# Performance work log

Measured on AMD Instinct MI355X. Metric: run time of the kernel, lower is better.

The kernel has to match this reference:

```python
import jax, jax.numpy as jnp
import numpy as np

B, S, OBS, ZD, HID, T, PD = 256, 512, 64, 16, 256, 64, 2
ITERS, ELITES = 4, 64
SMOOTH, STD_FLOOR = 0.25, 0.2
IW, AW, RW = 1.0, 0.5, 1.0


def setup_inputs() -> dict:
    key = jax.random.key(0)
    ks = jax.random.split(key, 32)
    f32 = jnp.float32

    def w(k, shape):
        return jax.random.normal(k, shape, f32) / np.float32(np.sqrt(shape[0]))

    return {
        "s0": jax.random.normal(ks[0], (B, OBS), f32),
        "eps": jax.random.normal(ks[1], (ITERS, B, S, ZD), f32),
        "enc_w1": w(ks[2], (OBS, HID)), "enc_b1": jnp.zeros((HID,), f32),
        "enc_w2": w(ks[3], (HID, HID)), "enc_b2": jnp.zeros((HID,), f32),
        "zmu_w": w(ks[4], (HID, ZD)), "zmu_b": jnp.zeros((ZD,), f32),
        "zls_w": w(ks[5], (HID, ZD)), "zls_b": jnp.zeros((ZD,), f32),
        "mu_w1": w(ks[6], (OBS + ZD, HID)), "mu_b1": jnp.zeros((HID,), f32),
        "mu_w2": w(ks[7], (HID, HID)), "mu_b2": jnp.zeros((HID,), f32),
        "mu_w3": w(ks[8], (HID, T * PD)), "mu_b3": jnp.zeros((T * PD,), f32),
        "sig_w1": w(ks[9], (ZD, HID)), "sig_b1": jnp.zeros((HID,), f32),
        "sig_w2": w(ks[10], (HID, HID)), "sig_b2": jnp.zeros((HID,), f32),
        "sig_w3": w(ks[11], (HID, T * PD)), "sig_b3": jnp.zeros((T * PD,), f32),  # bias zero-init per nn.init.zeros_
        "risk_w1": w(ks[12], (OBS + ZD, HID)), "risk_b1": jnp.zeros((HID,), f32),
        "risk_w2": w(ks[13], (HID, HID)), "risk_b2": jnp.zeros((HID,), f32),
        "risk_w3": w(ks[14], (HID, 1)), "risk_b3": jnp.zeros((1,), f32),
    }


def _cem_bind(s0, eps, enc_w1, enc_b1, enc_w2, enc_b2, zmu_w, zmu_b, zls_w, zls_b,
              mu_w1, mu_b1, mu_w2, mu_b2, mu_w3, mu_b3,
              sig_w1, sig_b1, sig_w2, sig_b2, sig_w3, sig_b3,
              risk_w1, risk_b1, risk_w2, risk_b2, risk_w3, risk_b3):
    relu = jax.nn.relu
    b, obs = s0.shape
    iters, _, s, zd = eps.shape

    # --- TubeNet.encode: q(z|s0) ---
    h = relu(s0 @ enc_w1 + enc_b1)
    h = relu(h @ enc_w2 + enc_b2)
    mu = h @ zmu_w + zmu_b                                   # [B, ZD]
    std = jnp.exp(jnp.clip(h @ zls_w + zls_b, -4.0, 2.0))    # [B, ZD]

    goal = s0[:, 2:4]                                        # extract_goal
    s0e = jnp.broadcast_to(s0[:, None, :], (b, s, obs))      # [B, S, OBS]

    best_score = jnp.full((b,), -jnp.inf, dtype=s0.dtype)
    best_z = mu

    for i in range(iters):  # small fixed CEM iteration count
        z = mu[:, None, :] + std[:, None, :] * eps[i]        # [B, S, ZD]
        x = jnp.concatenate([s0e, z], axis=-1)               # [B, S, OBS+ZD]

        # predict_tube: mu_net(s0, z)
        hm = relu(x @ mu_w1 + mu_b1)
        hm = relu(hm @ mu_w2 + mu_b2)
        mu_out = (hm @ mu_w3 + mu_b3).reshape(b, s, T, PD)

        # sigma_net(z), clamp(-4, 3); agency = -mean(log sigma) = -mean(logsig)
        hs = relu(z @ sig_w1 + sig_b1)
        hs = relu(hs @ sig_w2 + sig_b2)
        logsig = jnp.clip(hs @ sig_w3 + sig_b3, -4.0, 3.0)   # [B, S, T*PD]

        # intent proxy: ||mu_T - goal||^2
        intent = jnp.sum((mu_out[:, :, -1, :] - goal[:, None, :]) ** 2, axis=-1)  # [B, S]
        agency = -jnp.mean(logsig, axis=-1)                  # [B, S]

        # RiskNet(s0, z)
        hr = relu(x @ risk_w1 + risk_b1)
        hr = relu(hr @ risk_w2 + risk_b2)
        risk = jax.nn.sigmoid(hr @ risk_w3 + risk_b3)[..., 0]  # [B, S]

        score = -IW * intent + AW * agency - RW * risk       # [B, S]

        vals, idx = jax.lax.top_k(score, ELITES)             # [B, E]
        elite_z = jnp.take_along_axis(z, idx[:, :, None], axis=1)  # [B, E, ZD]

        better = vals[:, 0] > best_score
        top_z = jnp.take_along_axis(z, idx[:, :1, None], axis=1)[:, 0, :]
        best_score = jnp.where(better, vals[:, 0], best_score)
        best_z = jnp.where(better[:, None], top_z, best_z)

        new_mu = elite_z.mean(axis=1)
        new_std = jnp.std(elite_z, axis=1, ddof=1)           # torch .std default (unbiased)
        mu = SMOOTH * mu + (1.0 - SMOOTH) * new_mu
        std = jnp.maximum(SMOOTH * std + (1.0 - SMOOTH) * new_std, STD_FLOOR)

    return jnp.concatenate([best_z, best_score[:, None]], axis=-1)  # [B, ZD+1]


def reference(s0, eps, enc_w1, enc_b1, enc_w2, enc_b2, zmu_w, zmu_b, zls_w, zls_b,
              mu_w1, mu_b1, mu_w2, mu_b2, mu_w3, mu_b3,
              sig_w1, sig_b1, sig_w2, sig_b2, sig_w3, sig_b3,
              risk_w1, risk_b1, risk_w2, risk_b2, risk_w3, risk_b3):
    return _cem_bind(s0, eps, enc_w1, enc_b1, enc_w2, enc_b2, zmu_w, zmu_b, zls_w, zls_b,
                     mu_w1, mu_b1, mu_w2, mu_b2, mu_w3, mu_b3,
                     sig_w1, sig_b1, sig_w2, sig_b2, sig_w3, sig_b3,
                     risk_w1, risk_b1, risk_w2, risk_b2, risk_w3, risk_b3)
```

## Files before the change

kernel.cpp:

```cpp
#include <hip/hip_runtime.h>

#define B_    256
#define S_    512
#define OBS_  64
#define ZD_   16
#define HID_  256
#define ITERS_ 4
#define RT_   16
#define STR_  20

__global__ __launch_bounds__(256) void enc_kernel(
    const float* __restrict__ s0,
    const float* __restrict__ w1, const float* __restrict__ b1,
    const float* __restrict__ w2, const float* __restrict__ b2,
    const float* __restrict__ zmw, const float* __restrict__ zmb,
    const float* __restrict__ zlw, const float* __restrict__ zlb,
    const float* __restrict__ mu_w1, const float* __restrict__ mu_b1,
    const float* __restrict__ risk_w1, const float* __restrict__ risk_b1,
    float* __restrict__ mu, float* __restrict__ stdv, float* __restrict__ bscore,
    float* __restrict__ base_mu, float* __restrict__ base_risk)
{
    __shared__ float s0s[OBS_];
    __shared__ float h1[HID_];
    __shared__ float h2[HID_];
    const int b = blockIdx.x, tid = threadIdx.x;
    if (tid < OBS_) s0s[tid] = s0[b * OBS_ + tid];
    __syncthreads();
    {
        float am = mu_b1[tid], ar = risk_b1[tid];
        for (int k = 0; k < OBS_; ++k) {
            am = fmaf(s0s[k], mu_w1[k * 256 + tid], am);
            ar = fmaf(s0s[k], risk_w1[k * 256 + tid], ar);
        }
        base_mu[b * 256 + tid]   = am;
        base_risk[b * 256 + tid] = ar;
    }
    float a = b1[tid];
    for (int k = 0; k < OBS_; ++k) a = fmaf(s0s[k], w1[k * HID_ + tid], a);
    h1[tid] = fmaxf(a, 0.f);
    __syncthreads();
    float a2 = b2[tid];
    for (int k = 0; k < HID_; ++k) a2 = fmaf(h1[k], w2[k * HID_ + tid], a2);
    h2[tid] = fmaxf(a2, 0.f);
    __syncthreads();
    if (tid < ZD_) {
        float m = zmb[tid];
        for (int k = 0; k < HID_; ++k) m = fmaf(h2[k], zmw[k * ZD_ + tid], m);
        mu[b * ZD_ + tid] = m;
    } else if (tid < 2 * ZD_) {
        const int d = tid - ZD_;
        float l = zlb[d];
        for (int k = 0; k < HID_; ++k) l = fmaf(h2[k], zlw[k * ZD_ + d], l);
        l = fminf(fmaxf(l, -4.f), 2.f);
        stdv[b * ZD_ + d] = expf(l);
    } else if (tid == 2 * ZD_) {
        bscore[b] = -INFINITY;
    }
}

__device__ __forceinline__ void fma16x2(
    const float* __restrict__ row, float wx, float wy,
    float* __restrict__ acc0, float* __restrict__ acc1)
{
    const float4 a0 = *(const float4*)(row);
    const float4 a1 = *(const float4*)(row + 4);
    const float4 a2 = *(const float4*)(row + 8);
    const float4 a3 = *(const float4*)(row + 12);
    const float aa[16] = {a0.x,a0.y,a0.z,a0.w, a1.x,a1.y,a1.z,a1.w,
                          a2.x,a2.y,a2.z,a2.w, a3.x,a3.y,a3.z,a3.w};
#pragma unroll
    for (int r = 0; r < 16; ++r) {
        acc0[r] = fmaf(aa[r], wx, acc0[r]);
        acc1[r] = fmaf(aa[r], wy, acc1[r]);
    }
}

__device__ __forceinline__ void fma16x1(
    const float* __restrict__ row, float w, float* __restrict__ acc)
{
    const float4 a0 = *(const float4*)(row);
    const float4 a1 = *(const float4*)(row + 4);
    const float4 a2 = *(const float4*)(row + 8);
    const float4 a3 = *(const float4*)(row + 12);
    const float aa[16] = {a0.x,a0.y,a0.z,a0.w, a1.x,a1.y,a1.z,a1.w,
                          a2.x,a2.y,a2.z,a2.w, a3.x,a3.y,a3.z,a3.w};
#pragma unroll
    for (int r = 0; r < 16; ++r) acc[r] = fmaf(aa[r], w, acc[r]);
}

__device__ __forceinline__ void gemm_k2(
    const float* __restrict__ inS, int K,
    const float* __restrict__ wcol,
    float* __restrict__ acc0, float* __restrict__ acc1)
{
    float2 wA[4], wB[4];
#pragma unroll
    for (int i = 0; i < 4; ++i) wA[i] = *(const float2*)(wcol + (size_t)i * 256);
#pragma unroll 1
    for (int k0 = 0; k0 < K; k0 += 8) {
#pragma unroll
        for (int i = 0; i < 4; ++i)
            wB[i] = *(const float2*)(wcol + (size_t)(k0 + 4 + i) * 256);
#pragma unroll
        for (int i = 0; i < 4; ++i)
            fma16x2(inS + (k0 + i) * STR_, wA[i].x, wA[i].y, acc0, acc1);
        if (k0 + 8 < K) {
#pragma unroll
            for (int i = 0; i < 4; ++i)
                wA[i] = *(const float2*)(wcol + (size_t)(k0 + 8 + i) * 256);
        }
#pragma unroll
        for (int i = 0; i < 4; ++i)
            fma16x2(inS + (k0 + 4 + i) * STR_, wB[i].x, wB[i].y, acc0, acc1);
    }
}

__device__ __forceinline__ void gemm_k1(
    const float* __restrict__ inS, int K,
    const float* __restrict__ wcol, int wstride, float* __restrict__ acc)
{
    float wA[4], wB[4];
#pragma unroll
    for (int i = 0; i < 4; ++i) wA[i] = wcol[(size_t)i * wstride];
#pragma unroll 1
    for (int k0 = 0; k0 < K; k0 += 8) {
#pragma unroll
        for (int i = 0; i < 4; ++i) wB[i] = wcol[(size_t)(k0 + 4 + i) * wstride];
#pragma unroll
        for (int i = 0; i < 4; ++i) fma16x1(inS + (k0 + i) * STR_, wA[i], acc);
        if (k0 + 8 < K) {
#pragma unroll
            for (int i = 0; i < 4; ++i) wA[i] = wcol[(size_t)(k0 + 8 + i) * wstride];
        }
#pragma unroll
        for (int i = 0; i < 4; ++i) fma16x1(inS + (k0 + 4 + i) * STR_, wB[i], acc);
    }
}

__device__ __forceinline__ void store16_relu(float* __restrict__ dst, int c,
                                             const float* __restrict__ acc)
{
#pragma unroll
    for (int q = 0; q < 4; ++q) {
        float4 o;
        o.x = fmaxf(acc[4*q+0], 0.f); o.y = fmaxf(acc[4*q+1], 0.f);
        o.z = fmaxf(acc[4*q+2], 0.f); o.w = fmaxf(acc[4*q+3], 0.f);
        *(float4*)(dst + (size_t)c * STR_ + 4*q) = o;
    }
}

__global__ __launch_bounds__(128) void score_kernel(
    const float* __restrict__ s0, const float* __restrict__ eps,
    const float* __restrict__ mu_w1,
    const float* __restrict__ mu_w2, const float* __restrict__ mu_b2,
    const float* __restrict__ mu_w3, const float* __restrict__ mu_b3,
    const float* __restrict__ sig_w1, const float* __restrict__ sig_b1,
    const float* __restrict__ sig_w2, const float* __restrict__ sig_b2,
    const float* __restrict__ sig_w3, const float* __restrict__ sig_b3,
    const float* __restrict__ risk_w1,
    const float* __restrict__ risk_w2, const float* __restrict__ risk_b2,
    const float* __restrict__ risk_w3, const float* __restrict__ risk_b3,
    const float* __restrict__ base_mu, const float* __restrict__ base_risk,
    const float* __restrict__ mu, const float* __restrict__ stdv,
    float* __restrict__ score, int iter)
{
    __shared__ __align__(16) float zT[ZD_ * STR_];
    __shared__ __align__(16) float h[HID_ * STR_];
    __shared__ float w3m[2 * HID_];
    __shared__ float rw3[HID_];
    __shared__ float red[8][RT_], red2[8][RT_];
    __shared__ float intentL[RT_], agencyL[RT_];
    __shared__ float muS[ZD_], stdS[ZD_];

    const int tid  = threadIdx.x;
    const int c0   = tid * 2;
    const int row0 = blockIdx.x * RT_;
    const int b    = row0 >> 9;

    if (tid < ZD_) { muS[tid] = mu[b * ZD_ + tid]; stdS[tid] = stdv[b * ZD_ + tid]; }
    for (int l = tid; l < HID_; l += 128) {
        const float2 v = *(const float2*)(mu_w3 + (size_t)l * 128 + 126);
        w3m[2 * l] = v.x; w3m[2 * l + 1] = v.y;
        rw3[l] = risk_w3[l];
    }
    __syncthreads();
    {
        const float* epsI = eps + ((size_t)iter * B_ * S_ + row0) * ZD_;
        for (int l = tid; l < RT_ * ZD_; l += 128) {
            const int r = l >> 4, d = l & 15;
            zT[d * STR_ + r] = fmaf(stdS[d], epsI[l], muS[d]);
        }
    }
    __syncthreads();

    float acc0[RT_], acc1[RT_];

    {
        const float2 bm = *(const float2*)(base_mu + (size_t)b * 256 + c0);
#pragma unroll
        for (int r = 0; r < RT_; ++r) { acc0[r] = bm.x; acc1[r] = bm.y; }
        gemm_k2(zT, ZD_, mu_w1 + (size_t)OBS_ * 256 + c0, acc0, acc1);
        store16_relu(h, c0, acc0); store16_relu(h, c0 + 1, acc1);
    }
    __syncthreads();
    {
        const float2 bv = *(const float2*)(mu_b2 + c0);
#pragma unroll
        for (int r = 0; r < RT_; ++r) { acc0[r] = bv.x; acc1[r] = bv.y; }
        gemm_k2(h, HID_, mu_w2 + c0, acc0, acc1);
    }
    __syncthreads();
    store16_relu(h, c0, acc0); store16_relu(h, c0 + 1, acc1);
    __syncthreads();
    {
        const int r = tid & 15, seg = tid >> 4;
        float p0 = 0.f, p1 = 0.f;
        for (int i = 0; i < 32; ++i) {
            const int k = seg * 32 + i;
            const float hv = h[k * STR_ + r];
            p0 = fmaf(hv, w3m[2 * k],     p0);
            p1 = fmaf(hv, w3m[2 * k + 1], p1);
        }
        red[seg][r] = p0; red2[seg][r] = p1;
    }
    {
        const float2 bv = *(const float2*)(sig_b1 + c0);
#pragma unroll
        for (int r = 0; r < RT_; ++r) { acc0[r] = bv.x; acc1[r] = bv.y; }
        gemm_k2(zT, ZD_, sig_w1 + c0, acc0, acc1);
    }
    __syncthreads();
    store16_relu(h, c0, acc0); store16_relu(h, c0 + 1, acc1);
    if (tid < RT_) {
        float m0 = 0.f, m1 = 0.f;
#pragma unroll
        for (int sg = 0; sg < 8; ++sg) { m0 += red[sg][tid]; m1 += red2[sg][tid]; }
        m0 += mu_b3[126]; m1 += mu_b3[127];
        const float g0 = s0[b * OBS_ + 2], g1 = s0[b * OBS_ + 3];
        const float d0 = m0 - g0, d1 = m1 - g1;
        intentL[tid] = d0 * d0 + d1 * d1;
    }
    __syncthreads();
    {
        const float2 bv = *(const float2*)(sig_b2 + c0);
#pragma unroll
        for (int r = 0; r < RT_; ++r) { acc0[r] = bv.x; acc1[r] = bv.y; }
        gemm_k2(h, HID_, sig_w2 + c0, acc0, acc1);
    }
    __syncthreads();
    store16_relu(h, c0, acc0); store16_relu(h, c0 + 1, acc1);
    __syncthreads();
    {
        float acc[RT_];
        const float bv = sig_b3[tid];
#pragma unroll
        for (int r = 0; r < RT_; ++r) acc[r] = bv;
        gemm_k1(h, HID_, sig_w3 + tid, 128, acc);
        __syncthreads();
#pragma unroll
        for (int q = 0; q < 4; ++q) {
            float4 o;
            o.x = fminf(fmaxf(acc[4*q+0], -4.f), 3.f);
            o.y = fminf(fmaxf(acc[4*q+1], -4.f), 3.f);
            o.z = fminf(fmaxf(acc[4*q+2], -4.f), 3.f);
            o.w = fminf(fmaxf(acc[4*q+3], -4.f), 3.f);
            *(float4*)(h + (size_t)tid * STR_ + 4*q) = o;
        }
    }
    __syncthreads();
    {
        const int r = tid & 15, seg = tid >> 4;
        float s = 0.f;
        for (int i = 0; i < 16; ++i) s += h[(seg * 16 + i) * STR_ + r];
        red[seg][r] = s;
    }
    {
        const float2 bm = *(const float2*)(base_risk + (size_t)b * 256 + c0);
#pragma unroll
        for (int r = 0; r < RT_; ++r) { acc0[r] = bm.x; acc1[r] = bm.y; }
        gemm_k2(zT, ZD_, risk_w1 + (size_t)OBS_ * 256 + c0, acc0, acc1);
    }
    __syncthreads();
    store16_relu(h, c0, acc0); store16_relu(h, c0 + 1, acc1);
    if (tid < RT_) {
        float s = 0.f;
#pragma unroll
        for (int sg = 0; sg < 8; ++sg) s += red[sg][tid];
        agencyL[tid] = -s * (1.f / 128.f);
    }
    __syncthreads();
    {
        const float2 bv = *(const float2*)(risk_b2 + c0);
#pragma unroll
        for (int r = 0; r < RT_; ++r) { acc0[r] = bv.x; acc1[r] = bv.y; }
        gemm_k2(h, HID_, risk_w2 + c0, acc0, acc1);
    }
    __syncthreads();
    store16_relu(h, c0, acc0); store16_relu(h, c0 + 1, acc1);
    __syncthreads();
    {
        const int r = tid & 15, seg = tid >> 4;
        float p = 0.f;
        for (int i = 0; i < 32; ++i) {
            const int k = seg * 32 + i;
            p = fmaf(h[k * STR_ + r], rw3[k], p);
        }
        red[seg][r] = p;
    }
    __syncthreads();
    if (tid < RT_) {
        float p = 0.f;
#pragma unroll
        for (int sg = 0; sg < 8; ++sg) p += red[sg][tid];
        const float risk = 1.f / (1.f + expf(-(p + risk_b3[0])));
        score[row0 + tid] = -intentL[tid] + 0.5f * agencyL[tid] - risk;
    }
}

__global__ __launch_bounds__(256) void update_kernel(
    const float* __restrict__ score, const float* __restrict__ eps,
    float* __restrict__ mu, float* __restrict__ stdv,
    float* __restrict__ bscore, float* __restrict__ bz, int iter)
{
    __shared__ unsigned long long keys[512];
    __shared__ float ez[64][ZD_];
    __shared__ float mold[ZD_], sold[ZD_];
    __shared__ int flagL, idx0L;

    const int b = blockIdx.x, tid = threadIdx.x;

    for (int l = tid; l < 512; l += 256) {
        const float sc = score[b * 512 + l];
        unsigned int u = __float_as_uint(sc);
        u = (u & 0x80000000u) ? ~u : (u | 0x80000000u);
        const unsigned long long key =
            ((unsigned long long)u << 32) | (unsigned long long)(511 - l);
        keys[l] = ~key;
    }
    if (tid < ZD_) { mold[tid] = mu[b * ZD_ + tid]; sold[tid] = stdv[b * ZD_ + tid]; }
    __syncthreads();

    for (int size = 2; size < 512; size <<= 1) {
        const int ddd = ((tid & (size >> 1)) != 0) ? 0 : 1;
        for (int stride = size >> 1; stride > 0; stride >>= 1) {
            __syncthreads();
            const int pos = 2 * tid - (tid & (stride - 1));
            const unsigned long long a = keys[pos], c = keys[pos + stride];
            if ((a > c) == (ddd != 0)) { keys[pos] = c; keys[pos + stride] = a; }
        }
    }
    for (int stride = 256; stride > 0; stride >>= 1) {
        __syncthreads();
        const int pos = 2 * tid - (tid & (stride - 1));
        const unsigned long long a = keys[pos], c = keys[pos + stride];
        if (a > c) { keys[pos] = c; keys[pos + stride] = a; }
    }
    __syncthreads();

    const float* epsB = eps + ((size_t)iter * B_ * S_ + (size_t)b * S_) * ZD_;
    for (int l = tid; l < 64 * ZD_; l += 256) {
        const int e = l >> 4, d = l & 15;
        const unsigned long long key = ~keys[e];
        const int idx = 511 - (int)(key & 0xFFFFFFFFull);
        ez[e][d] = fmaf(sold[d], epsB[idx * ZD_ + d], mold[d]);
    }
    __syncthreads();

    if (tid < ZD_) {
        float s = 0.f;
        for (int e = 0; e < 64; ++e) s += ez[e][tid];
        const float mean = s * (1.f / 64.f);
        float v = 0.f;
        for (int e = 0; e < 64; ++e) { const float d = ez[e][tid] - mean; v = fmaf(d, d, v); }
        const float sd = sqrtf(v * (1.f / 63.f));
        mu[b * ZD_ + tid]   = 0.25f * mold[tid] + 0.75f * mean;
        stdv[b * ZD_ + tid] = fmaxf(0.25f * sold[tid] + 0.75f * sd, 0.2f);
    }
    if (tid == 0) {
        const unsigned long long key = ~keys[0];
        const int idx0 = 511 - (int)(key & 0xFFFFFFFFull);
        const float v = score[b * 512 + idx0];
        const int better = (v > bscore[b]) ? 1 : 0;
        if (better) bscore[b] = v;
        flagL = better; idx0L = idx0;
    }
    __syncthreads();
    if (tid < ZD_ && flagL)
        bz[b * ZD_ + tid] = fmaf(sold[tid], epsB[idx0L * ZD_ + tid], mold[tid]);
}

__global__ __launch_bounds__(256) void out_kernel(
    const float* __restrict__ bz, const float* __restrict__ bscore,
    float* __restrict__ out)
{
    const int i = blockIdx.x * 256 + threadIdx.x;
    if (i < B_ * 17) {
        const int b = i / 17, d = i % 17;
        out[i] = (d < ZD_) ? bz[b * ZD_ + d] : bscore[b];
    }
}

extern "C" void kernel_launch(void* const* d_in, const int* in_sizes, int n_in,
                              void* d_out, int out_size, void* d_ws, size_t ws_size,
                              hipStream_t stream)
{
    (void)in_sizes; (void)n_in; (void)out_size; (void)ws_size;
    const float* s0      = (const float*)d_in[0];
    const float* eps     = (const float*)d_in[1];
    const float* enc_w1  = (const float*)d_in[2];
    const float* enc_b1  = (const float*)d_in[3];
    const float* enc_w2  = (const float*)d_in[4];
    const float* enc_b2  = (const float*)d_in[5];
    const float* zmu_w   = (const float*)d_in[6];
    const float* zmu_b   = (const float*)d_in[7];
    const float* zls_w   = (const float*)d_in[8];
    const float* zls_b   = (const float*)d_in[9];
    const float* mu_w1   = (const float*)d_in[10];
    const float* mu_b1   = (const float*)d_in[11];
    const float* mu_w2   = (const float*)d_in[12];
    const float* mu_b2   = (const float*)d_in[13];
    const float* mu_w3   = (const float*)d_in[14];
    const float* mu_b3   = (const float*)d_in[15];
    const float* sig_w1  = (const float*)d_in[16];
    const float* sig_b1  = (const float*)d_in[17];
    const float* sig_w2  = (const float*)d_in[18];
    const float* sig_b2  = (const float*)d_in[19];
    const float* sig_w3  = (const float*)d_in[20];
    const float* sig_b3  = (const float*)d_in[21];
    const float* risk_w1 = (const float*)d_in[22];
    const float* risk_b1 = (const float*)d_in[23];
    const float* risk_w2 = (const float*)d_in[24];
    const float* risk_b2 = (const float*)d_in[25];
    const float* risk_w3 = (const float*)d_in[26];
    const float* risk_b3 = (const float*)d_in[27];

    float* ws        = (float*)d_ws;
    float* mu        = ws;
    float* stdv      = ws + 4096;
    float* bscore    = ws + 8192;
    float* bz        = ws + 8448;
    float* score     = ws + 12544;
    float* base_mu   = ws + 143616;
    float* base_risk = ws + 209152;

    enc_kernel<<<B_, 256, 0, stream>>>(s0, enc_w1, enc_b1, enc_w2, enc_b2,
                                       zmu_w, zmu_b, zls_w, zls_b,
                                       mu_w1, mu_b1, risk_w1, risk_b1,
                                       mu, stdv, bscore, base_mu, base_risk);
    for (int it = 0; it < ITERS_; ++it) {
        score_kernel<<<(B_ * S_) / RT_, 128, 0, stream>>>(
            s0, eps,
            mu_w1, mu_w2, mu_b2, mu_w3, mu_b3,
            sig_w1, sig_b1, sig_w2, sig_b2, sig_w3, sig_b3,
            risk_w1, risk_w2, risk_b2, risk_w3, risk_b3,
            base_mu, base_risk,
            mu, stdv, score, it);
        update_kernel<<<B_, 256, 0, stream>>>(score, eps, mu, stdv, bscore, bz, it);
    }
    out_kernel<<<(B_ * 17 + 255) / 256, 256, 0, stream>>>(bz, bscore,
                                                          (float*)d_out);
}
```

Before: 3.527 ms.

## Double row tile to 32 per block with two 128-thread row groups

Each score block now handles 32 sample rows using 256 threads split into two groups of 128. Each group computes 16 rows against the same weight columns, so weight loads per row are roughly halved across the block. Shared staging of the w3 and risk_w3 vectors is dropped in favour of direct global reads, and the reductions use a cross-lane shuffle before writing partial sums. The shared h buffer grows with the larger stride, which may limit how many blocks fit per CU, and the launch bounds now request four blocks.

```diff
diff --git a/kernel.cpp b/kernel.cpp
--- a/kernel.cpp
+++ b/kernel.cpp
@@ -6,8 +6,8 @@
 #define ZD_   16
 #define HID_  256
 #define ITERS_ 4
-#define RT_   16
-#define STR_  20
+#define RT_   32
+#define STRH_ 36
 
 __global__ __launch_bounds__(256) void enc_kernel(
     const float* __restrict__ s0,
@@ -103,7 +103,7 @@
             wB[i] = *(const float2*)(wcol + (size_t)(k0 + 4 + i) * 256);
 #pragma unroll
         for (int i = 0; i < 4; ++i)
-            fma16x2(inS + (k0 + i) * STR_, wA[i].x, wA[i].y, acc0, acc1);
+            fma16x2(inS + (k0 + i) * STRH_, wA[i].x, wA[i].y, acc0, acc1);
         if (k0 + 8 < K) {
 #pragma unroll
             for (int i = 0; i < 4; ++i)
@@ -111,7 +111,7 @@
         }
 #pragma unroll
         for (int i = 0; i < 4; ++i)
-            fma16x2(inS + (k0 + 4 + i) * STR_, wB[i].x, wB[i].y, acc0, acc1);
+            fma16x2(inS + (k0 + 4 + i) * STRH_, wB[i].x, wB[i].y, acc0, acc1);
     }
 }
 
@@ -127,29 +127,29 @@
 #pragma unroll
         for (int i = 0; i < 4; ++i) wB[i] = wcol[(size_t)(k0 + 4 + i) * wstride];
 #pragma unroll
-        for (int i = 0; i < 4; ++i) fma16x1(inS + (k0 + i) * STR_, wA[i], acc);
+        for (int i = 0; i < 4; ++i) fma16x1(inS + (k0 + i) * STRH_, wA[i], acc);
         if (k0 + 8 < K) {
 #pragma unroll
             for (int i = 0; i < 4; ++i) wA[i] = wcol[(size_t)(k0 + 8 + i) * wstride];
         }
 #pragma unroll
-        for (int i = 0; i < 4; ++i) fma16x1(inS + (k0 + 4 + i) * STR_, wB[i], acc);
+        for (int i = 0; i < 4; ++i) fma16x1(inS + (k0 + 4 + i) * STRH_, wB[i], acc);
     }
 }
 
 __device__ __forceinline__ void store16_relu(float* __restrict__ dst, int c,
-                                             const float* __restrict__ acc)
+                                             int g16, const float* __restrict__ acc)
 {
 #pragma unroll
     for (int q = 0; q < 4; ++q) {
         float4 o;
         o.x = fmaxf(acc[4*q+0], 0.f); o.y = fmaxf(acc[4*q+1], 0.f);
         o.z = fmaxf(acc[4*q+2], 0.f); o.w = fmaxf(acc[4*q+3], 0.f);
-        *(float4*)(dst + (size_t)c * STR_ + 4*q) = o;
-    }
-}
-
-__global__ __launch_bounds__(128) void score_kernel(
+        *(float4*)(dst + (size_t)c * STRH_ + g16 + 4*q) = o;
+    }
+}
+
+__global__ __launch_bounds__(256, 4) void score_kernel(
     const float* __restrict__ s0, const float* __restrict__ eps,
     const float* __restrict__ mu_w1,
     const float* __restrict__ mu_w2, const float* __restrict__ mu_b2,
@@ -164,78 +164,74 @@
     const float* __restrict__ mu, const float* __restrict__ stdv,
     float* __restrict__ score, int iter)
 {
-    __shared__ __align__(16) float zT[ZD_ * STR_];
-    __shared__ __align__(16) float h[HID_ * STR_];
-    __shared__ float w3m[2 * HID_];
-    __shared__ float rw3[HID_];
-    __shared__ float red[8][RT_], red2[8][RT_];
+    __shared__ __align__(16) float zT[ZD_ * STRH_];
+    __shared__ __align__(16) float h[HID_ * STRH_];
+    __shared__ float red[4][RT_], red2[4][RT_];
     __shared__ float intentL[RT_], agencyL[RT_];
     __shared__ float muS[ZD_], stdS[ZD_];
 
     const int tid  = threadIdx.x;
-    const int c0   = tid * 2;
+    const int g    = tid >> 7;
+    const int g16  = g * 16;
+    const int c0   = (tid & 127) * 2;
     const int row0 = blockIdx.x * RT_;
     const int b    = row0 >> 9;
 
     if (tid < ZD_) { muS[tid] = mu[b * ZD_ + tid]; stdS[tid] = stdv[b * ZD_ + tid]; }
-    for (int l = tid; l < HID_; l += 128) {
-        const float2 v = *(const float2*)(mu_w3 + (size_t)l * 128 + 126);
-        w3m[2 * l] = v.x; w3m[2 * l + 1] = v.y;
-        rw3[l] = risk_w3[l];
-    }
     __syncthreads();
     {
         const float* epsI = eps + ((size_t)iter * B_ * S_ + row0) * ZD_;
-        for (int l = tid; l < RT_ * ZD_; l += 128) {
-            const int r = l >> 4, d = l & 15;
-            zT[d * STR_ + r] = fmaf(stdS[d], epsI[l], muS[d]);
-        }
-    }
-    __syncthreads();
-
-    float acc0[RT_], acc1[RT_];
+        for (int l = tid; l < RT_ * ZD_; l += 256) {
+            const int r = l & 31, d = l >> 5;
+            zT[d * STRH_ + r] = fmaf(stdS[d], epsI[r * ZD_ + d], muS[d]);
+        }
+    }
+    __syncthreads();
+
+    float acc0[16], acc1[16];
 
     {
         const float2 bm = *(const float2*)(base_mu + (size_t)b * 256 + c0);
 #pragma unroll
-        for (int r = 0; r < RT_; ++r) { acc0[r] = bm.x; acc1[r] = bm.y; }
-        gemm_k2(zT, ZD_, mu_w1 + (size_t)OBS_ * 256 + c0, acc0, acc1);
-        store16_relu(h, c0, acc0); store16_relu(h, c0 + 1, acc1);
+        for (int r = 0; r < 16; ++r) { acc0[r] = bm.x; acc1[r] = bm.y; }
+        gemm_k2(zT + g16, ZD_, mu_w1 + (size_t)OBS_ * 256 + c0, acc0, acc1);
+        store16_relu(h, c0, g16, acc0); store16_relu(h, c0 + 1, g16, acc1);
     }
     __syncthreads();
     {
         const float2 bv = *(const float2*)(mu_b2 + c0);
 #pragma unroll
-        for (int r = 0; r < RT_; ++r) { acc0[r] = bv.x; acc1[r] = bv.y; }
-        gemm_k2(h, HID_, mu_w2 + c0, acc0, acc1);
-    }
-    __syncthreads();
-    store16_relu(h, c0, acc0); store16_relu(h, c0 + 1, acc1);
-    __syncthreads();
-    {
-        const int r = tid & 15, seg = tid >> 4;
+        for (int r = 0; r < 16; ++r) { acc0[r] = bv.x; acc1[r] = bv.y; }
+        gemm_k2(h + g16, HID_, mu_w2 + c0, acc0, acc1);
+    }
+    __syncthreads();
+    store16_relu(h, c0, g16, acc0); store16_relu(h, c0 + 1, g16, acc1);
+    __syncthreads();
+    {
+        const int r = tid & 31, seg = tid >> 5, w = tid >> 6;
         float p0 = 0.f, p1 = 0.f;
         for (int i = 0; i < 32; ++i) {
             const int k = seg * 32 + i;
-            const float hv = h[k * STR_ + r];
-            p0 = fmaf(hv, w3m[2 * k],     p0);
-            p1 = fmaf(hv, w3m[2 * k + 1], p1);
-        }
-        red[seg][r] = p0; red2[seg][r] = p1;
+            const float hv = h[k * STRH_ + r];
+            const float2 wv = *(const float2*)(mu_w3 + (size_t)k * 128 + 126);
+            p0 = fmaf(hv, wv.x, p0);
+            p1 = fmaf(hv, wv.y, p1);
+        }
+        p0 += __shfl_xor(p0, 32);
+        p1 += __shfl_xor(p1, 32);
+        if ((tid & 32) == 0) { red[w][r] = p0; red2[w][r] = p1; }
     }
     {
         const float2 bv = *(const float2*)(sig_b1 + c0);
 #pragma unroll
-        for (int r = 0; r < RT_; ++r) { acc0[r] = bv.x; acc1[r] = bv.y; }
-        gemm_k2(zT, ZD_, sig_w1 + c0, acc0, acc1);
-    }
-    __syncthreads();
-    store16_relu(h, c0, acc0); store16_relu(h, c0 + 1, acc1);
+        for (int r = 0; r < 16; ++r) { acc0[r] = bv.x; acc1[r] = bv.y; }
+        gemm_k2(zT + g16, ZD_, sig_w1 + c0, acc0, acc1);
+    }
+    __syncthreads();
+    store16_relu(h, c0, g16, acc0); store16_relu(h, c0 + 1, g16, acc1);
     if (tid < RT_) {
-        float m0 = 0.f, m1 = 0.f;
-#pragma unroll
-        for (int sg = 0; sg < 8; ++sg) { m0 += red[sg][tid]; m1 += red2[sg][tid]; }
-        m0 += mu_b3[126]; m1 += mu_b3[127];
+        float m0 = red[0][tid] + red[1][tid] + red[2][tid] + red[3][tid] + mu_b3[126];
+        float m1 = red2[0][tid] + red2[1][tid] + red2[2][tid] + red2[3][tid] + mu_b3[127];
         const float g0 = s0[b * OBS_ + 2], g1 = s0[b * OBS_ + 3];
         const float d0 = m0 - g0, d1 = m1 - g1;
         intentL[tid] = d0 * d0 + d1 * d1;
@@ -244,18 +240,19 @@
     {
         const float2 bv = *(const float2*)(sig_b2 + c0);
 #pragma unroll
-        for (int r = 0; r < RT_; ++r) { acc0[r] = bv.x; acc1[r] = bv.y; }
-        gemm_k2(h, HID_, sig_w2 + c0, acc0, acc1);
-    }
-    __syncthreads();
-    store16_relu(h, c0, acc0); store16_relu(h, c0 + 1, acc1);
-    __syncthreads();
-    {
-        float acc[RT_];
-        const float bv = sig_b3[tid];
-#pragma unroll
-        for (int r = 0; r < RT_; ++r) acc[r] = bv;
-        gemm_k1(h, HID_, sig_w3 + tid, 128, acc);
+        for (int r = 0; r < 16; ++r) { acc0[r] = bv.x; acc1[r] = bv.y; }
+        gemm_k2(h + g16, HID_, sig_w2 + c0, acc0, acc1);
+    }
+    __syncthreads();
+    store16_relu(h, c0, g16, acc0); store16_relu(h, c0 + 1, g16, acc1);
+    __syncthreads();
+    {
+        const int c = tid & 127;
+        float acc[16];
+        const float bv = sig_b3[c];
+#pragma unroll
+        for (int r = 0; r < 16; ++r) acc[r] = bv;
+        gemm_k1(h + g16, HID_, sig_w3 + c, 128, acc);
         __syncthreads();
 #pragma unroll
         for (int q = 0; q < 4; ++q) {
@@ -264,54 +261,52 @@
             o.y = fminf(fmaxf(acc[4*q+1], -4.f), 3.f);
             o.z = fminf(fmaxf(acc[4*q+2], -4.f), 3.f);
             o.w = fminf(fmaxf(acc[4*q+3], -4.f), 3.f);
-            *(float4*)(h + (size_t)tid * STR_ + 4*q) = o;
-        }
-    }
-    __syncthreads();
-    {
-        const int r = tid & 15, seg = tid >> 4;
+            *(float4*)(h + (size_t)c * STRH_ + g16 + 4*q) = o;
+        }
+    }
+    __syncthreads();
+    {
+        const int r = tid & 31, seg = tid >> 5, w = tid >> 6;
         float s = 0.f;
-        for (int i = 0; i < 16; ++i) s += h[(seg * 16 + i) * STR_ + r];
-        red[seg][r] = s;
+        for (int i = 0; i < 16; ++i) s += h[(seg * 16 + i) * STRH_ + r];
+        s += __shfl_xor(s, 32);
+        if ((tid & 32) == 0) red[w][r] = s;
     }
     {
         const float2 bm = *(const float2*)(base_risk + (size_t)b * 256 + c0);
 #pragma unroll
-        for (int r = 0; r < RT_; ++r) { acc0[r] = bm.x; acc1[r] = bm.y; }
-        gemm_k2(zT, ZD_, risk_w1 + (size_t)OBS_ * 256 + c0, acc0, acc1);
-    }
-    __syncthreads();
-    store16_relu(h, c0, acc0); store16_relu(h, c0 + 1, acc1);
+        for (int r = 0; r < 16; ++r) { acc0[r] = bm.x; acc1[r] = bm.y; }
+        gemm_k2(zT + g16, ZD_, risk_w1 + (size_t)OBS_ * 256 + c0, acc0, acc1);
+    }
+    __syncthreads();
+    store16_relu(h, c0, g16, acc0); store16_relu(h, c0 + 1, g16, acc1);
     if (tid < RT_) {
-        float s = 0.f;
-#pragma unroll
-        for (int sg = 0; sg < 8; ++sg) s += red[sg][tid];
+        const float s = red[0][tid] + red[1][tid] + red[2][tid] + red[3][tid];
         agencyL[tid] = -s * (1.f / 128.f);
     }
     __syncthreads();
     {
         const float2 bv = *(const float2*)(risk_b2 + c0);
 #pragma unroll
-        for (int r = 0; r < RT_; ++r) { acc0[r] = bv.x; acc1[r] = bv.y; }
-        gemm_k2(h, HID_, risk_w2 + c0, acc0, acc1);
-    }
-    __syncthreads();
-    store16_relu(h, c0, acc0); store16_relu(h, c0 + 1, acc1);
-    __syncthreads();
-    {
-        const int r = tid & 15, seg = tid >> 4;
+        for (int r = 0; r < 16; ++r) { acc0[r] = bv.x; acc1[r] = bv.y; }
+        gemm_k2(h + g16, HID_, risk_w2 + c0, acc0, acc1);
+    }
+    __syncthreads();
+    store16_relu(h, c0, g16, acc0); store16_relu(h, c0 + 1, g16, acc1);
+    __syncthreads();
+    {
+        const int r = tid & 31, seg = tid >> 5, w = tid >> 6;
         float p = 0.f;
         for (int i = 0; i < 32; ++i) {
             const int k = seg * 32 + i;
-            p = fmaf(h[k * STR_ + r], rw3[k], p);
-        }
-        red[seg][r] = p;
+            p = fmaf(h[k * STRH_ + r], risk_w3[k], p);
+        }
+        p += __shfl_xor(p, 32);
+        if ((tid & 32) == 0) red[w][r] = p;
     }
     __syncthreads();
     if (tid < RT_) {
-        float p = 0.f;
-#pragma unroll
-        for (int sg = 0; sg < 8; ++sg) p += red[sg][tid];
+        const float p = red[0][tid] + red[1][tid] + red[2][tid] + red[3][tid];
         const float risk = 1.f / (1.f + expf(-(p + risk_b3[0])));
         score[row0 + tid] = -intentL[tid] + 0.5f * agencyL[tid] - risk;
     }
@@ -448,7 +443,7 @@
                                        mu_w1, mu_b1, risk_w1, risk_b1,
                                        mu, stdv, bscore, base_mu, base_risk);
     for (int it = 0; it < ITERS_; ++it) {
-        score_kernel<<<(B_ * S_) / RT_, 128, 0, stream>>>(
+        score_kernel<<<(B_ * S_) / RT_, 256, 0, stream>>>(
             s0, eps,
             mu_w1, mu_w2, mu_b2, mu_w3, mu_b3,
             sig_w1, sig_b1, sig_w2, sig_b2, sig_w3, sig_b3,
```

New measurement: 3.330 ms. -5.6%, faster.
